# Performance work log

Measured on AMD Instinct MI355X. Metric: run time of the kernel, lower is better.

The kernel has to match this reference:

```python
import jax, jax.numpy as jnp
import numpy as np

B, IN_C, CH = 16384, 128, 512
EMBED_DIM = 6240          # = 64*64 + 64 + 64*32 + 32 (BatchDecoder param count)
NUM_EMB = 512
DEC_IN, DEC_H, DATA_Y = 64, 64, 32


def setup_inputs() -> dict:
    key = jax.random.key(0)
    ks = jax.random.split(key, 16)
    s = lambda fan_in: 1.0 / np.sqrt(fan_in)
    return {
        "x":   jax.random.normal(ks[0], (B, IN_C), jnp.float32),
        # enc_f: Linear(IN_C,CH) -> ReLU -> Linear(CH,EMBED_DIM)
        "Wf1": jax.random.normal(ks[1], (IN_C, CH), jnp.float32) * s(IN_C),
        "bf1": jax.random.normal(ks[2], (CH,), jnp.float32) * s(IN_C),
        "Wf2": jax.random.normal(ks[3], (CH, EMBED_DIM), jnp.float32) * s(CH),
        "bf2": jax.random.normal(ks[4], (EMBED_DIM,), jnp.float32) * s(CH),
        # enc_x: Linear(IN_C,CH) -> ReLU -> Linear(CH,DEC_IN)
        "Wx1": jax.random.normal(ks[5], (IN_C, CH), jnp.float32) * s(IN_C),
        "bx1": jax.random.normal(ks[6], (CH,), jnp.float32) * s(IN_C),
        "Wx2": jax.random.normal(ks[7], (CH, DEC_IN), jnp.float32) * s(CH),
        "bx2": jax.random.normal(ks[8], (DEC_IN,), jnp.float32) * s(CH),
        # VQ codebook: [dim, num_embeddings] as in Quantize
        "embed": jax.random.normal(ks[9], (EMBED_DIM, NUM_EMB), jnp.float32),
        # BatchDecoder per-codeword MLP parameters (nets' own init params;
        # the original's weight-injection loop is a no-op: `p = new_vec` only
        # rebinds a local, so the nets run with their initialized weights)
        "W1": jax.random.normal(ks[10], (NUM_EMB, DEC_IN, DEC_H), jnp.float32) * s(DEC_IN),
        "b1": jax.random.normal(ks[11], (NUM_EMB, DEC_H), jnp.float32) * s(DEC_IN),
        "W2": jax.random.normal(ks[12], (NUM_EMB, DEC_H, DATA_Y), jnp.float32) * s(DEC_H),
        "b2": jax.random.normal(ks[13], (NUM_EMB, DATA_Y), jnp.float32) * s(DEC_H),
    }


def reference(x, Wf1, bf1, Wf2, bf2, Wx1, bx1, Wx2, bx2, embed, W1, b1, W2, b2):
    # ---- encode: enc_f MLP -> [B, EMBED_DIM] ----
    pre_f = jax.nn.relu(x @ Wf1 + bf1) @ Wf2 + bf2
    # ---- Quantize (eval mode; EMA buffer updates are side effects only) ----
    # dist[b,k] = ||pre_f[b]||^2 - 2 pre_f[b].embed[:,k] + ||embed[:,k]||^2
    dist = (jnp.sum(pre_f * pre_f, axis=1, keepdims=True)
            - 2.0 * (pre_f @ embed)
            + jnp.sum(embed * embed, axis=0, keepdims=True))  # [B, K]
    embed_ind = jnp.argmin(dist, axis=1)                       # [B]
    encodings = jax.nn.one_hot(embed_ind, NUM_EMB, dtype=pre_f.dtype)
    quantize = embed.T[embed_ind]                              # [B, EMBED_DIM]
    diff = jnp.mean((jax.lax.stop_gradient(quantize) - pre_f) ** 2)
    z_q = pre_f + jax.lax.stop_gradient(quantize - pre_f)      # straight-through (unused by buggy decoder)
    avg_probs = jnp.mean(encodings, axis=0)
    perplexity = jnp.exp(-jnp.sum(avg_probs * jnp.log(avg_probs + 1e-10)))
    # ---- enc_x MLP -> [B, DEC_IN] ----
    embedded_x = jax.nn.relu(x @ Wx1 + bx1) @ Wx2 + bx2
    # ---- BatchDecoder: per-sample expert MLP dispatch by embed_ind ----
    h = jax.nn.relu(jnp.einsum('bi,bih->bh', embedded_x, W1[embed_ind]) + b1[embed_ind])
    dec = jnp.einsum('bh,bho->bo', h, W2[embed_ind]) + b2[embed_ind]  # [B, DATA_Y]
    return (dec, diff, embed_ind, perplexity)
```

## Files before the change

kernel.cpp:

```cpp
#include <hip/hip_runtime.h>
#include <math.h>

#define BN     16384
#define INC    128
#define CH     512
#define ED     6240
#define KN     512
#define DIN    64
#define DH     64
#define DY     32
#define NCW    195
#define CHP    (CH + 8)

#define OUT_DEC   0
#define OUT_DIFF  (BN*DY)
#define OUT_IND   (BN*DY + 1)
#define OUT_PERP  (BN*DY + 1 + BN)

typedef _Float16 half8 __attribute__((ext_vector_type(8)));
typedef float    f32x4 __attribute__((ext_vector_type(4)));
#define MFMA16(a, b, c) __builtin_amdgcn_mfma_f32_16x16x32_f16(a, b, c, 0, 0, 0)

__device__ __forceinline__ size_t paddr(int tile, int NC, int c, int lane, int e) {
    return ((size_t)(tile * NC + c) * 64 + lane) * 8 + e;
}

__global__ __launch_bounds__(256) void packall_kernel(
        const float* __restrict__ x,
        const float* __restrict__ Wf1, const float* __restrict__ Wx1,
        const float* __restrict__ bf1, const float* __restrict__ bx1,
        const float* __restrict__ Wx2,
        const float* __restrict__ Wf2, const float* __restrict__ bf2,
        const float* __restrict__ embed,
        _Float16* __restrict__ XPs, _Float16* __restrict__ XPl,
        _Float16* __restrict__ WfxPs, _Float16* __restrict__ WfxPl,
        float* __restrict__ bfx,
        _Float16* __restrict__ Wx2Ps, _Float16* __restrict__ Wx2Pl,
        _Float16* __restrict__ WfPs, _Float16* __restrict__ WfPl,
        _Float16* __restrict__ EmPs, _Float16* __restrict__ EmPl,
        float* __restrict__ s2p, float* __restrict__ bep,
        float* __restrict__ w0) {
    __shared__ __align__(16) char smem[16384];
    int id = blockIdx.x;
    int t = threadIdx.x;
    if (id < 12480) {
        float (*red)[33] = (float(*)[33])smem;
        int bx = id % NCW, by = id / NCW;
        int d = bx * 32 + (t & 31);
        int j = by * 8 + (t >> 5);
        float v = Wf2[(size_t)j * ED + d];
        _Float16 hi = (_Float16)v;
        size_t a = paddr(j >> 4, NCW, d >> 5, ((d & 31) >> 3) * 16 + (j & 15), d & 7);
        WfPs[a] = hi;
        WfPl[a] = (_Float16)(v - (float)hi);
        red[t >> 5][t & 31] = v * bf2[d];
        __syncthreads();
        if (t < 8) {
            float s = 0.f;
            #pragma unroll
            for (int i = 0; i < 32; ++i) s += red[t][i];
            atomicAdd(&w0[by * 8 + t], s);
        }
    } else if (id < 15600) {
        float (*tile)[33] = (float(*)[33])smem;
        int sub = id - 12480;
        int bx = sub % NCW, by = sub / NCW;
        int dl = t >> 5, kl = t & 31;
        #pragma unroll
        for (int r = 0; r < 4; ++r)
            tile[dl + 8 * r][kl] = embed[(size_t)(bx * 32 + dl + 8 * r) * KN
                                         + by * 32 + kl];
        __syncthreads();
        int d = bx * 32 + kl;
        #pragma unroll
        for (int r = 0; r < 4; ++r) {
            int k = by * 32 + dl + 8 * r;
            float v = tile[kl][dl + 8 * r];
            _Float16 hi = (_Float16)v;
            size_t a = paddr(k >> 4, NCW, d >> 5, ((d & 31) >> 3) * 16 + (k & 15), d & 7);
            EmPs[a] = hi;
            EmPl[a] = (_Float16)(v - (float)hi);
        }
    } else if (id < 15728) {
        float (*rs)[33] = (float(*)[33])smem;
        float (*rb)[33] = (float(*)[33])(smem + 8 * 33 * 4);
        int sub = id - 15600;
        int bx = sub % 16, by = sub / 16;
        int kl = t & 31, dl = t >> 5;
        int kb = bx * 32;
        int d0 = by * 780;
        float s = 0.f, b = 0.f;
        for (int d = d0 + dl; d < d0 + 780; d += 8) {
            float e = embed[(size_t)d * KN + kb + kl];
            s = fmaf(e, e, s);
            b = fmaf(bf2[d], e, b);
        }
        rs[dl][kl] = s; rb[dl][kl] = b;
        __syncthreads();
        if (t < 32) {
            float ss = 0.f, bb = 0.f;
            #pragma unroll
            for (int i = 0; i < 8; ++i) { ss += rs[i][t]; bb += rb[i][t]; }
            s2p[by * KN + kb + t] = ss;
            bep[by * KN + kb + t] = bb;
        }
    } else if (id < 16240) {
        float (*xt)[INC] = (float(*)[INC])smem;
        int m0 = (id - 15728) * 32;
        for (int i = t; i < 32 * (INC / 4); i += 256) {
            int row = i >> 5, c4 = (i & 31) << 2;
            *(float4*)&xt[row][c4] = *(const float4*)&x[(size_t)(m0 + row) * INC + c4];
        }
        __syncthreads();
        int ta = m0 >> 4;
        #pragma unroll
        for (int i = 0; i < 2; ++i) {
            int idx = t + 256 * i;
            int tile2 = idx >> 8;
            int c = (idx >> 6) & 3;
            int lane = idx & 63;
            int m = tile2 * 16 + (lane & 15);
            int d0 = c * 32 + ((lane >> 4) << 3);
            half8 hh, ll;
            #pragma unroll
            for (int e = 0; e < 8; ++e) {
                float v = xt[m][d0 + e];
                _Float16 hi = (_Float16)v;
                hh[e] = hi;
                ll[e] = (_Float16)(v - (float)hi);
            }
            *(half8*)(XPs + paddr(ta + tile2, 4, c, lane, 0)) = hh;
            *(half8*)(XPl + paddr(ta + tile2, 4, c, lane, 0)) = ll;
        }
    } else if (id < 16304) {
        int tile = id - 16240;
        for (int i = t; i < 2048; i += 256) {
            int c = i >> 9, lane = (i >> 3) & 63, e = i & 7;
            int n = tile * 16 + (lane & 15);
            int d = c * 32 + ((lane >> 4) << 3) + e;
            float v = (n < 512) ? Wf1[(size_t)d * CH + n] : Wx1[(size_t)d * CH + n - 512];
            _Float16 hi = (_Float16)v;
            size_t a = paddr(tile, 4, c, lane, e);
            WfxPs[a] = hi;
            WfxPl[a] = (_Float16)(v - (float)hi);
        }
        if (tile == 0)
            for (int j = t; j < 512; j += 256) { bfx[j] = bf1[j]; bfx[512 + j] = bx1[j]; }
    } else {
        int tile = id - 16304;
        for (int i = t; i < 8192; i += 256) {
            int c = i >> 9, lane = (i >> 3) & 63, e = i & 7;
            int n = tile * 16 + (lane & 15);
            int d = c * 32 + ((lane >> 4) << 3) + e;
            float v = Wx2[(size_t)d * DIN + n];
            _Float16 hi = (_Float16)v;
            size_t a = paddr(tile, 16, c, lane, e);
            Wx2Ps[a] = hi;
            Wx2Pl[a] = (_Float16)(v - (float)hi);
        }
    }
}

__global__ __launch_bounds__(512) void mfma_weg_kernel(
        const _Float16* __restrict__ WfPs, const _Float16* __restrict__ WfPl,
        const _Float16* __restrict__ EmPs, const _Float16* __restrict__ EmPl,
        float* __restrict__ WeP, float* __restrict__ GP) {
    int t = threadIdx.x;
    int w = t >> 6, L = t & 63;
    int lane16 = L & 15, quad = L >> 4;
    int m0 = blockIdx.x * 128 + (w & 3) * 32;
    int n0 = blockIdx.y * 128 + (w >> 2) * 64;
    int ta = m0 >> 4, tb = n0 >> 4;
    int zraw = blockIdx.z;
    bool isWe = zraw < 8;
    int z = isWe ? zraw : zraw - 8;
    int base = NCW / 8, rem = NCW % 8;
    int c0 = z * base + (z < rem ? z : rem);
    int cnt = base + (z < rem ? 1 : 0);
    f32x4 acc[2][4];
    #pragma unroll
    for (int rt = 0; rt < 2; ++rt)
        #pragma unroll
        for (int tt = 0; tt < 4; ++tt) acc[rt][tt] = (f32x4){0.f, 0.f, 0.f, 0.f};
    if (isWe) {
        for (int ci = 0; ci < cnt; ++ci) {
            int c = c0 + ci;
            size_t oa0 = paddr(ta, NCW, c, L, 0), oa1 = paddr(ta + 1, NCW, c, L, 0);
            half8 A0h = *(const half8*)(WfPs + oa0);
            half8 A0l = *(const half8*)(WfPl + oa0);
            half8 A1h = *(const half8*)(WfPs + oa1);
            half8 A1l = *(const half8*)(WfPl + oa1);
            #pragma unroll
            for (int tt = 0; tt < 4; ++tt) {
                size_t ob = paddr(tb + tt, NCW, c, L, 0);
                half8 Bh = *(const half8*)(EmPs + ob);
                half8 Bl8 = *(const half8*)(EmPl + ob);
                acc[0][tt] = MFMA16(A0h, Bl8, MFMA16(A0l, Bh, MFMA16(A0h, Bh, acc[0][tt])));
                acc[1][tt] = MFMA16(A1h, Bl8, MFMA16(A1l, Bh, MFMA16(A1h, Bh, acc[1][tt])));
            }
        }
    } else {
        for (int ci = 0; ci < cnt; ++ci) {
            int c = c0 + ci;
            half8 A0h = *(const half8*)(WfPs + paddr(ta, NCW, c, L, 0));
            half8 A1h = *(const half8*)(WfPs + paddr(ta + 1, NCW, c, L, 0));
            #pragma unroll
            for (int tt = 0; tt < 4; ++tt) {
                half8 Bh = *(const half8*)(WfPs + paddr(tb + tt, NCW, c, L, 0));
                acc[0][tt] = MFMA16(A0h, Bh, acc[0][tt]);
                acc[1][tt] = MFMA16(A1h, Bh, acc[1][tt]);
            }
        }
    }
    float* C = (isWe ? WeP : GP) + (size_t)z * KN * KN;
    #pragma unroll
    for (int rt = 0; rt < 2; ++rt)
        #pragma unroll
        for (int tt = 0; tt < 4; ++tt)
            #pragma unroll
            for (int r = 0; r < 4; ++r)
                C[(size_t)(m0 + rt * 16 + quad * 4 + r) * KN
                  + n0 + tt * 16 + lane16] = acc[rt][tt][r];
}

__global__ __launch_bounds__(256) void wepackgred_kernel(
        const float* __restrict__ WeP, const float* __restrict__ GP,
        const float* __restrict__ s2p, const float* __restrict__ bep,
        _Float16* __restrict__ WePs, _Float16* __restrict__ WePl,
        _Float16* __restrict__ GhPs, float* __restrict__ s2,
        float* __restrict__ be) {
    int id = blockIdx.x;
    int t = threadIdx.x;
    if (id < 1024) {
        int g = id * 256 + t;
        int j = g >> 9, k = g & 511;
        float v = 0.f;
        #pragma unroll
        for (int z = 0; z < 8; ++z) v += WeP[(size_t)z * KN * KN + g];
        _Float16 hi = (_Float16)v;
        size_t a = paddr(k >> 4, 16, j >> 5, ((j & 31) >> 3) * 16 + (k & 15), j & 7);
        WePs[a] = hi;
        WePl[a] = (_Float16)(v - (float)hi);
    } else if (id < 2048) {
        int g = (id - 1024) * 256 + t;
        int m = g >> 9, n = g & 511;
        float v = 0.f;
        #pragma unroll
        for (int z = 0; z < 8; ++z) v += GP[(size_t)z * KN * KN + g];
        GhPs[paddr(n >> 4, 16, m >> 5, ((m & 31) >> 3) * 16 + (n & 15), m & 7)]
            = (_Float16)v;
    } else {
        #pragma unroll
        for (int i = 0; i < 2; ++i) {
            int k = t + 256 * i;
            float s = 0.f, b = 0.f;
            #pragma unroll
            for (int y = 0; y < 8; ++y) {
                s += s2p[y * KN + k];
                b += bep[y * KN + k];
            }
            s2[k] = s;
            be[k] = b;
        }
    }
}

__global__ __launch_bounds__(512) void enc1_kernel(
        const _Float16* __restrict__ XPs, const _Float16* __restrict__ XPl,
        const _Float16* __restrict__ WfxPs, const _Float16* __restrict__ WfxPl,
        const float* __restrict__ bfx,
        const _Float16* __restrict__ Wx2Ps, const _Float16* __restrict__ Wx2Pl,
        const float* __restrict__ bx2,
        const _Float16* __restrict__ WePs, const _Float16* __restrict__ WePl,
        const _Float16* __restrict__ GhPs,
        const float* __restrict__ s2, const float* __restrict__ be,
        float* __restrict__ colsum,
        float* __restrict__ EX,
        int* __restrict__ ind, float* __restrict__ out_ind,
        int* __restrict__ counts, float* __restrict__ diffsum) {
    __shared__ _Float16 hhi[32][CHP];
    __shared__ _Float16 hlo[32][CHP];
    __shared__ float redv[8][32];
    __shared__ int   redi[8][32];
    __shared__ float fin[32];
    __shared__ float gpart[8];
    int t = threadIdx.x;
    int w = t >> 6, L = t & 63;
    int l16 = L & 15, quad = L >> 4;
    int m0 = blockIdx.x * 32;
    int ta = m0 >> 4;
    int enc = blockIdx.y;
    int n0 = enc * 512 + w * 64;
    int tb = n0 >> 4;
    f32x4 acc[2][4];
    #pragma unroll
    for (int rt = 0; rt < 2; ++rt)
        #pragma unroll
        for (int tt = 0; tt < 4; ++tt) acc[rt][tt] = (f32x4){0.f, 0.f, 0.f, 0.f};
    #pragma unroll
    for (int c = 0; c < 4; ++c) {
        size_t oa0 = paddr(ta, 4, c, L, 0), oa1 = paddr(ta + 1, 4, c, L, 0);
        half8 A0h = *(const half8*)(XPs + oa0);
        half8 A0l = *(const half8*)(XPl + oa0);
        half8 A1h = *(const half8*)(XPs + oa1);
        half8 A1l = *(const half8*)(XPl + oa1);
        #pragma unroll
        for (int tt = 0; tt < 4; ++tt) {
            size_t ob = paddr(tb + tt, 4, c, L, 0);
            half8 Bh = *(const half8*)(WfxPs + ob);
            half8 Bl8 = *(const half8*)(WfxPl + ob);
            acc[0][tt] = MFMA16(A0h, Bl8, MFMA16(A0l, Bh, MFMA16(A0h, Bh, acc[0][tt])));
            acc[1][tt] = MFMA16(A1h, Bl8, MFMA16(A1l, Bh, MFMA16(A1h, Bh, acc[1][tt])));
        }
    }
    #pragma unroll
    for (int rt = 0; rt < 2; ++rt)
        #pragma unroll
        for (int tt = 0; tt < 4; ++tt) {
            int col = w * 64 + tt * 16 + l16;
            float bias = bfx[enc * 512 + col];
            #pragma unroll
            for (int r = 0; r < 4; ++r) {
                int row = rt * 16 + quad * 4 + r;
                float v = fmaxf(acc[rt][tt][r] + bias, 0.f);
                _Float16 hi = (_Float16)v;
                hhi[row][col] = hi;
                hlo[row][col] = (_Float16)(v - (float)hi);
            }
        }
    __syncthreads();
    if (enc == 0) {
        float s = 0.f;
        #pragma unroll
        for (int r = 0; r < 32; ++r) s += (float)hhi[r][t] + (float)hlo[r][t];
        atomicAdd(&colsum[t], s);
        int colbase = w * 64;
        int tbs = w * 4;
        float cks[4];
        #pragma unroll
        for (int tt = 0; tt < 4; ++tt) {
            int c = colbase + tt * 16 + l16;
            cks[tt] = 0.5f * s2[c] - be[c];
        }
        #pragma unroll
        for (int rt = 0; rt < 2; ++rt)
            #pragma unroll
            for (int tt = 0; tt < 4; ++tt) acc[rt][tt] = (f32x4){0.f, 0.f, 0.f, 0.f};
        for (int c = 0; c < 16; ++c) {
            int d0 = c * 32 + (quad << 3);
            int mA0 = l16, mA1 = 16 + l16;
            half8 A0h = *(const half8*)(&hhi[mA0][d0]);
            half8 A0l = *(const half8*)(&hlo[mA0][d0]);
            half8 A1h = *(const half8*)(&hhi[mA1][d0]);
            half8 A1l = *(const half8*)(&hlo[mA1][d0]);
            #pragma unroll
            for (int tt = 0; tt < 4; ++tt) {
                size_t ob = paddr(tbs + tt, 16, c, L, 0);
                half8 Bh = *(const half8*)(WePs + ob);
                half8 Bl8 = *(const half8*)(WePl + ob);
                acc[0][tt] = MFMA16(A0h, Bl8, MFMA16(A0l, Bh, MFMA16(A0h, Bh, acc[0][tt])));
                acc[1][tt] = MFMA16(A1h, Bl8, MFMA16(A1l, Bh, MFMA16(A1h, Bh, acc[1][tt])));
            }
        }
        #pragma unroll
        for (int rt = 0; rt < 2; ++rt) {
            #pragma unroll
            for (int r = 0; r < 4; ++r) {
                float mv = cks[0] - acc[rt][0][r];
                int mi = colbase + l16;
                #pragma unroll
                for (int tt = 1; tt < 4; ++tt) {
                    float v = cks[tt] - acc[rt][tt][r];
                    int c = colbase + tt * 16 + l16;
                    if (v < mv || (v == mv && c < mi)) { mv = v; mi = c; }
                }
                #pragma unroll
                for (int d = 1; d < 16; d <<= 1) {
                    float ov = __shfl_xor(mv, d);
                    int oi = __shfl_xor(mi, d);
                    if (ov < mv || (ov == mv && oi < mi)) { mv = ov; mi = oi; }
                }
                if (l16 == 0) {
                    int row = rt * 16 + quad * 4 + r;
                    redv[w][row] = mv; redi[w][row] = mi;
                }
            }
        }
        #pragma unroll
        for (int rt = 0; rt < 2; ++rt)
            #pragma unroll
            for (int tt = 0; tt < 4; ++tt) acc[rt][tt] = (f32x4){0.f, 0.f, 0.f, 0.f};
        for (int c = 0; c < 16; ++c) {
            int d0 = c * 32 + (quad << 3);
            half8 A0h = *(const half8*)(&hhi[l16][d0]);
            half8 A1h = *(const half8*)(&hhi[16 + l16][d0]);
            #pragma unroll
            for (int tt = 0; tt < 4; ++tt) {
                half8 Bh = *(const half8*)(GhPs + paddr(tbs + tt, 16, c, L, 0));
                acc[0][tt] = MFMA16(A0h, Bh, acc[0][tt]);
                acc[1][tt] = MFMA16(A1h, Bh, acc[1][tt]);
            }
        }
        float gs = 0.f;
        #pragma unroll
        for (int rt = 0; rt < 2; ++rt)
            #pragma unroll
            for (int tt = 0; tt < 4; ++tt) {
                int col = colbase + tt * 16 + l16;
                #pragma unroll
                for (int r = 0; r < 4; ++r) {
                    int row = rt * 16 + quad * 4 + r;
                    gs += acc[rt][tt][r] * (float)hhi[row][col];
                }
            }
        #pragma unroll
        for (int d = 1; d < 64; d <<= 1) gs += __shfl_xor(gs, d);
        if (L == 0) gpart[w] = gs;
        __syncthreads();
        if (t < 32) {
            float mv = redv[0][t]; int mi = redi[0][t];
            #pragma unroll
            for (int w2 = 1; w2 < 8; ++w2) {
                float ov = redv[w2][t]; int oi = redi[w2][t];
                if (ov < mv || (ov == mv && oi < mi)) { mv = ov; mi = oi; }
            }
            int b = m0 + t;
            ind[b] = mi;
            out_ind[b] = (float)mi;
            atomicAdd(&counts[mi], 1);
            fin[t] = 2.f * mv;
        }
        __syncthreads();
        if (t == 0) {
            float s = 0.f;
            #pragma unroll
            for (int i = 0; i < 32; ++i) s += fin[i];
            #pragma unroll
            for (int w2 = 0; w2 < 8; ++w2) s += gpart[w2];
            atomicAdd(diffsum, s);
        }
    } else {
        int rt = w & 1, ct = w >> 1;
        f32x4 eacc = (f32x4){0.f, 0.f, 0.f, 0.f};
        for (int c = 0; c < 16; ++c) {
            int d0 = c * 32 + (quad << 3);
            int m = rt * 16 + l16;
            half8 Ah = *(half8*)(&hhi[m][d0]);
            half8 Al = *(half8*)(&hlo[m][d0]);
            size_t ob = paddr(ct, 16, c, L, 0);
            half8 Bh = *(const half8*)(Wx2Ps + ob);
            half8 Bl8 = *(const half8*)(Wx2Pl + ob);
            eacc = MFMA16(Ah, Bl8, MFMA16(Al, Bh, MFMA16(Ah, Bh, eacc)));
        }
        int col = ct * 16 + l16;
        float bias = bx2[col];
        #pragma unroll
        for (int r = 0; r < 4; ++r) {
            int row = m0 + rt * 16 + quad * 4 + r;
            EX[(size_t)row * DIN + col] = eacc[r] + bias;
        }
    }
}

__global__ __launch_bounds__(512) void finalize_kernel(const int* __restrict__ counts,
                                                       const float* __restrict__ diffsum,
                                                       const float* __restrict__ colsum,
                                                       const float* __restrict__ w0,
                                                       const float* __restrict__ bf2,
                                                       float* __restrict__ out_diff,
                                                       float* __restrict__ out_perp) {
    __shared__ float sf[512];
    int t = threadIdx.x;
    int c = counts[t];
    double p = (double)c / (double)BN;
    double term = -p * log(p + 1e-10);
    float dotp = colsum[t] * w0[t];
    float bbp = 0.f;
    for (int d = t; d < ED; d += 512) { float v = bf2[d]; bbp = fmaf(v, v, bbp); }
    sf[t] = dotp; __syncthreads();
    for (int s = 256; s > 0; s >>= 1) { if (t < s) sf[t] += sf[t + s]; __syncthreads(); }
    float dot_all = sf[0];
    __syncthreads();
    sf[t] = bbp; __syncthreads();
    for (int s = 256; s > 0; s >>= 1) { if (t < s) sf[t] += sf[t + s]; __syncthreads(); }
    float bb = sf[0];
    __syncthreads();
    sf[t] = (float)term; __syncthreads();
    for (int s = 256; s > 0; s >>= 1) { if (t < s) sf[t] += sf[t + s]; __syncthreads(); }
    if (t == 0) {
        *out_perp = expf(sf[0]);
        *out_diff = (diffsum[0] + 2.f * dot_all + (float)BN * bb) /
                    ((float)BN * (float)ED);
    }
}

__global__ __launch_bounds__(256) void scatter_kernel(const int* __restrict__ ind,
                                                      const int* __restrict__ counts,
                                                      int* __restrict__ cursors,
                                                      int* __restrict__ perm) {
    __shared__ int sc[KN], soff[KN], lcount[KN], lbase[KN], lcur[KN];
    int t = threadIdx.x;
    for (int i = t; i < KN; i += 256) {
        sc[i] = counts[i];
        lcount[i] = 0; lcur[i] = 0;
    }
    __syncthreads();
    #pragma unroll
    for (int half = 0; half < 2; ++half) {
        int i = t + 256 * half;
        int off = 0;
        for (int k = 0; k < i; ++k) off += sc[k];
        soff[i] = off;
    }
    int b = blockIdx.x * 256 + t;
    int k = ind[b];
    atomicAdd(&lcount[k], 1);
    __syncthreads();
    for (int i = t; i < KN; i += 256) {
        int c = lcount[i];
        if (c > 0) lbase[i] = atomicAdd(&cursors[i], c);
    }
    __syncthreads();
    int pos = soff[k] + lbase[k] + atomicAdd(&lcur[k], 1);
    perm[pos] = b;
}

__global__ __launch_bounds__(256) void decode_kernel(const float* __restrict__ EX,
                                                     const int* __restrict__ perm,
                                                     const int* __restrict__ ind,
                                                     const float* __restrict__ W1,
                                                     const float* __restrict__ b1,
                                                     const float* __restrict__ W2,
                                                     const float* __restrict__ b2,
                                                     float* __restrict__ dec) {
    __shared__ float exs[4][DIN];
    __shared__ float h2s[4][DH];
    int t = threadIdx.x;
    int w = t >> 6, l = t & 63;
    int s = blockIdx.x * 4 + w;
    int b = perm[s];
    int k = ind[b];
    exs[w][l] = EX[(size_t)b * DIN + l];
    __syncthreads();
    const float* w1 = W1 + (size_t)k * (DIN * DH);
    float h = b1[(size_t)k * DH + l];
    #pragma unroll
    for (int j = 0; j < DIN; ++j)
        h = fmaf(exs[w][j], w1[(size_t)j * DH + l], h);
    h2s[w][l] = fmaxf(h, 0.f);
    __syncthreads();
    if (l < DY) {
        const float* w2 = W2 + (size_t)k * (DH * DY);
        float d = b2[(size_t)k * DY + l];
        #pragma unroll
        for (int j = 0; j < DH; ++j)
            d = fmaf(h2s[w][j], w2[(size_t)j * DY + l], d);
        dec[(size_t)b * DY + l] = d;
    }
}

extern "C" void kernel_launch(void* const* d_in, const int* in_sizes, int n_in,
                              void* d_out, int out_size, void* d_ws, size_t ws_size,
                              hipStream_t stream) {
    const float* x     = (const float*)d_in[0];
    const float* Wf1   = (const float*)d_in[1];
    const float* bf1   = (const float*)d_in[2];
    const float* Wf2   = (const float*)d_in[3];
    const float* bf2   = (const float*)d_in[4];
    const float* Wx1   = (const float*)d_in[5];
    const float* bx1   = (const float*)d_in[6];
    const float* Wx2   = (const float*)d_in[7];
    const float* bx2   = (const float*)d_in[8];
    const float* embed = (const float*)d_in[9];
    const float* W1    = (const float*)d_in[10];
    const float* b1    = (const float*)d_in[11];
    const float* W2    = (const float*)d_in[12];
    const float* b2    = (const float*)d_in[13];
    float* out = (float*)d_out;

    char* ws = (char*)d_ws;
    size_t off = 0;
    auto carve = [&](size_t bytes) -> void* {
        void* p = ws + off;
        off += (bytes + 255) & ~(size_t)255;
        return p;
    };
    _Float16* XPs   = (_Float16*)carve((size_t)BN * INC * 2);
    _Float16* XPl   = (_Float16*)carve((size_t)BN * INC * 2);
    _Float16* WfxPs = (_Float16*)carve((size_t)1024 * INC * 2);
    _Float16* WfxPl = (_Float16*)carve((size_t)1024 * INC * 2);
    float*    bfx   = (float*)carve(1024 * 4);
    _Float16* Wx2Ps = (_Float16*)carve((size_t)DIN * CH * 2);
    _Float16* Wx2Pl = (_Float16*)carve((size_t)DIN * CH * 2);
    _Float16* WfPs  = (_Float16*)carve((size_t)CH * ED * 2);
    _Float16* WfPl  = (_Float16*)carve((size_t)CH * ED * 2);
    _Float16* EmPs  = (_Float16*)carve((size_t)KN * ED * 2);
    _Float16* EmPl  = (_Float16*)carve((size_t)KN * ED * 2);
    char* un = (char*)carve((size_t)BN * CH * 2);
    float*    WeP = (float*)un;
    float*    GP  = (float*)(un + (size_t)8 * KN * KN * 4);
    _Float16* WePs = (_Float16*)carve((size_t)KN * CH * 2);
    _Float16* WePl = (_Float16*)carve((size_t)KN * CH * 2);
    _Float16* GhPs = (_Float16*)carve((size_t)KN * KN * 2);
    float*    EX   = (float*)carve((size_t)BN * DIN * 4);
    float*    s2p  = (float*)carve(8 * KN * 4);
    float*    bep  = (float*)carve(8 * KN * 4);
    float*    s2   = (float*)carve(KN * 4);
    float*    be   = (float*)carve(KN * 4);
    char* zbase = ws + off;
    float* w0    = (float*)carve(CH * 4);
    float* colsum= (float*)carve(CH * 4);
    int*   counts= (int*)carve(KN * 4);
    int*   cursors=(int*)carve(KN * 4);
    float* diffsum=(float*)carve(256);
    size_t zbytes = (size_t)(ws + off - zbase);
    int*   ind     = (int*)carve(BN * 4);
    int*   perm    = (int*)carve(BN * 4);
    (void)in_sizes; (void)n_in; (void)out_size; (void)ws_size;

    hipMemsetAsync(zbase, 0, zbytes, stream);
    packall_kernel<<<16308, 256, 0, stream>>>(x, Wf1, Wx1, bf1, bx1, Wx2, Wf2, bf2,
                                              embed, XPs, XPl, WfxPs, WfxPl, bfx,
                                              Wx2Ps, Wx2Pl, WfPs, WfPl, EmPs, EmPl,
                                              s2p, bep, w0);
    mfma_weg_kernel<<<dim3(4, 4, 16), 512, 0, stream>>>(WfPs, WfPl, EmPs, EmPl,
                                                        WeP, GP);
    wepackgred_kernel<<<2049, 256, 0, stream>>>(WeP, GP, s2p, bep,
                                                WePs, WePl, GhPs, s2, be);
    enc1_kernel<<<dim3(BN / 32, 2), 512, 0, stream>>>(XPs, XPl, WfxPs, WfxPl, bfx,
                                                      Wx2Ps, Wx2Pl, bx2,
                                                      WePs, WePl, GhPs, s2, be,
                                                      colsum, EX,
                                                      ind, out + OUT_IND, counts,
                                                      diffsum);
    scatter_kernel<<<BN / 256, 256, 0, stream>>>(ind, counts, cursors, perm);
    decode_kernel<<<BN / 4, 256, 0, stream>>>(EX, perm, ind, W1, b1, W2, b2,
                                              out + OUT_DEC);
    finalize_kernel<<<1, 512, 0, stream>>>(counts, diffsum, colsum, w0, bf2,
                                           out + OUT_DIFF, out + OUT_PERP);
}
```

Before: 339.7 us.

## Fuse Gram-matrix MFMA pass into distance loop and reorder enc1 grid

Merges the second MFMA loop over the hidden tile (computing the G-quadratic term) into the distance-GEMM loop, so the A fragments are read from shared memory once and one loop is removed. Column sums are now taken from register partials with wave shuffles instead of a 32-row shared-memory scan. The grid is transposed so both encoder halves of the same row tile run next to each other, and launch bounds request 4 waves per SIMD. The extra gcc accumulators raise register pressure, which may conflict with the occupancy hint and cause spills.

```diff
diff --git a/kernel.cpp b/kernel.cpp
--- a/kernel.cpp
+++ b/kernel.cpp
@@ -265,7 +265,7 @@
     }
 }
 
-__global__ __launch_bounds__(512) void enc1_kernel(
+__global__ __launch_bounds__(512, 4) void enc1_kernel(
         const _Float16* __restrict__ XPs, const _Float16* __restrict__ XPl,
         const _Float16* __restrict__ WfxPs, const _Float16* __restrict__ WfxPl,
         const float* __restrict__ bfx,
@@ -287,9 +287,9 @@
     int t = threadIdx.x;
     int w = t >> 6, L = t & 63;
     int l16 = L & 15, quad = L >> 4;
-    int m0 = blockIdx.x * 32;
+    int enc = blockIdx.x;
+    int m0 = blockIdx.y * 32;
     int ta = m0 >> 4;
-    int enc = blockIdx.y;
     int n0 = enc * 512 + w * 64;
     int tb = n0 >> 4;
     f32x4 acc[2][4];
@@ -313,6 +313,7 @@
             acc[1][tt] = MFMA16(A1h, Bl8, MFMA16(A1l, Bh, MFMA16(A1h, Bh, acc[1][tt])));
         }
     }
+    float colp[4] = {0.f, 0.f, 0.f, 0.f};
     #pragma unroll
     for (int rt = 0; rt < 2; ++rt)
         #pragma unroll
@@ -326,14 +327,18 @@
                 _Float16 hi = (_Float16)v;
                 hhi[row][col] = hi;
                 hlo[row][col] = (_Float16)(v - (float)hi);
+                colp[tt] += v;
             }
         }
     __syncthreads();
     if (enc == 0) {
-        float s = 0.f;
-        #pragma unroll
-        for (int r = 0; r < 32; ++r) s += (float)hhi[r][t] + (float)hlo[r][t];
-        atomicAdd(&colsum[t], s);
+        #pragma unroll
+        for (int tt = 0; tt < 4; ++tt) {
+            float s = colp[tt];
+            s += __shfl_xor(s, 16);
+            s += __shfl_xor(s, 32);
+            if (quad == 0) atomicAdd(&colsum[w * 64 + tt * 16 + l16], s);
+        }
         int colbase = w * 64;
         int tbs = w * 4;
         float cks[4];
@@ -342,24 +347,34 @@
             int c = colbase + tt * 16 + l16;
             cks[tt] = 0.5f * s2[c] - be[c];
         }
+        f32x4 gcc[2][4];
         #pragma unroll
         for (int rt = 0; rt < 2; ++rt)
             #pragma unroll
-            for (int tt = 0; tt < 4; ++tt) acc[rt][tt] = (f32x4){0.f, 0.f, 0.f, 0.f};
+            for (int tt = 0; tt < 4; ++tt) {
+                acc[rt][tt] = (f32x4){0.f, 0.f, 0.f, 0.f};
+                gcc[rt][tt] = (f32x4){0.f, 0.f, 0.f, 0.f};
+            }
+        const _Float16* hA0 = &hhi[l16][quad << 3];
+        const _Float16* lA0 = &hlo[l16][quad << 3];
+        const _Float16* hA1 = &hhi[16 + l16][quad << 3];
+        const _Float16* lA1 = &hlo[16 + l16][quad << 3];
         for (int c = 0; c < 16; ++c) {
-            int d0 = c * 32 + (quad << 3);
-            int mA0 = l16, mA1 = 16 + l16;
-            half8 A0h = *(const half8*)(&hhi[mA0][d0]);
-            half8 A0l = *(const half8*)(&hlo[mA0][d0]);
-            half8 A1h = *(const half8*)(&hhi[mA1][d0]);
-            half8 A1l = *(const half8*)(&hlo[mA1][d0]);
+            int d0 = c * 32;
+            half8 A0h = *(const half8*)(hA0 + d0);
+            half8 A0l = *(const half8*)(lA0 + d0);
+            half8 A1h = *(const half8*)(hA1 + d0);
+            half8 A1l = *(const half8*)(lA1 + d0);
             #pragma unroll
             for (int tt = 0; tt < 4; ++tt) {
                 size_t ob = paddr(tbs + tt, 16, c, L, 0);
                 half8 Bh = *(const half8*)(WePs + ob);
                 half8 Bl8 = *(const half8*)(WePl + ob);
+                half8 Gh = *(const half8*)(GhPs + ob);
                 acc[0][tt] = MFMA16(A0h, Bl8, MFMA16(A0l, Bh, MFMA16(A0h, Bh, acc[0][tt])));
                 acc[1][tt] = MFMA16(A1h, Bl8, MFMA16(A1l, Bh, MFMA16(A1h, Bh, acc[1][tt])));
+                gcc[0][tt] = MFMA16(A0h, Gh, gcc[0][tt]);
+                gcc[1][tt] = MFMA16(A1h, Gh, gcc[1][tt]);
             }
         }
         #pragma unroll
@@ -386,21 +401,6 @@
                 }
             }
         }
-        #pragma unroll
-        for (int rt = 0; rt < 2; ++rt)
-            #pragma unroll
-            for (int tt = 0; tt < 4; ++tt) acc[rt][tt] = (f32x4){0.f, 0.f, 0.f, 0.f};
-        for (int c = 0; c < 16; ++c) {
-            int d0 = c * 32 + (quad << 3);
-            half8 A0h = *(const half8*)(&hhi[l16][d0]);
-            half8 A1h = *(const half8*)(&hhi[16 + l16][d0]);
-            #pragma unroll
-            for (int tt = 0; tt < 4; ++tt) {
-                half8 Bh = *(const half8*)(GhPs + paddr(tbs + tt, 16, c, L, 0));
-                acc[0][tt] = MFMA16(A0h, Bh, acc[0][tt]);
-                acc[1][tt] = MFMA16(A1h, Bh, acc[1][tt]);
-            }
-        }
         float gs = 0.f;
         #pragma unroll
         for (int rt = 0; rt < 2; ++rt)
@@ -410,7 +410,7 @@
                 #pragma unroll
                 for (int r = 0; r < 4; ++r) {
                     int row = rt * 16 + quad * 4 + r;
-                    gs += acc[rt][tt][r] * (float)hhi[row][col];
+                    gs += gcc[rt][tt][r] * (float)hhi[row][col];
                 }
             }
         #pragma unroll
@@ -627,7 +627,7 @@
                                                         WeP, GP);
     wepackgred_kernel<<<2049, 256, 0, stream>>>(WeP, GP, s2p, bep,
                                                 WePs, WePl, GhPs, s2, be);
-    enc1_kernel<<<dim3(BN / 32, 2), 512, 0, stream>>>(XPs, XPl, WfxPs, WfxPl, bfx,
+    enc1_kernel<<<dim3(2, BN / 32), 512, 0, stream>>>(XPs, XPl, WfxPs, WfxPl, bfx,
                                                       Wx2Ps, Wx2Pl, bx2,
                                                       WePs, WePl, GhPs, s2, be,
                                                       colsum, EX,
```

New measurement: 350.1 us. 3.1% more time.
